# Performance work log

Measured on AMD Instinct MI355X. Metric: run time of the kernel, lower is better.

Reference implementation:

```python
import jax, jax.numpy as jnp
import numpy as np

N_EMBED = 384
HEAD_SIZE = 64
B, T = 128, 512


def rope(x):
    # Faithful to source: fres = 1/1000**(arange(0,dim,2)//dim) -> integer
    # floor-div makes the exponent all zeros, so fres == 1 everywhere.
    Bx, Tx, D = x.shape
    half = D // 2
    fres = jnp.ones((half,), dtype=jnp.float32)
    ang = jnp.arange(Tx, dtype=jnp.float32)[:, None] * fres[None, :]  # (T, half)
    cos, sin = jnp.cos(ang), jnp.sin(ang)
    xr = x.reshape(Bx, Tx, half, 2)
    xe, xo = xr[..., 0], xr[..., 1]
    oe = xe * cos - xo * sin
    oo = xe * sin + xo * cos
    return jnp.stack([oe, oo], axis=-1).reshape(Bx, Tx, D)


def setup_inputs() -> dict:
    key = jax.random.key(0)
    ks = jax.random.split(key, 7)
    s = 1.0 / np.sqrt(N_EMBED)
    return {
        "x": jax.random.normal(ks[0], (B, T, N_EMBED), dtype=jnp.float32),
        "wq": jax.random.uniform(ks[1], (N_EMBED, HEAD_SIZE), jnp.float32, -s, s),
        "bq": jax.random.uniform(ks[2], (HEAD_SIZE,), jnp.float32, -s, s),
        "wk": jax.random.uniform(ks[3], (N_EMBED, HEAD_SIZE), jnp.float32, -s, s),
        "bk": jax.random.uniform(ks[4], (HEAD_SIZE,), jnp.float32, -s, s),
        "wv": jax.random.uniform(ks[5], (N_EMBED, HEAD_SIZE), jnp.float32, -s, s),
        "bv": jax.random.uniform(ks[6], (HEAD_SIZE,), jnp.float32, -s, s),
    }


def reference(x, wq, bq, wk, bk, wv, bv):
    Bx, Tx, C = x.shape  # C = n_embed; scale uses C per the source (not head_size)
    q = rope(x @ wq + bq)
    k = rope(x @ wk + bk)
    wei = jnp.einsum("bqd,bkd->bqk", q, k) * (C ** -0.5)  # (B, T, T)
    causal = jnp.tril(jnp.ones((Tx, Tx), dtype=bool))
    wei = jnp.where(causal, wei, -jnp.inf)
    wei = jax.nn.softmax(wei, axis=-1)
    v = x @ wv + bv
    return jnp.einsum("bqk,bkd->bqd", wei, v)
```

## Files before the change

### kernel.cpp

```cpp
#include <hip/hip_runtime.h>

#define TSEQ 512
#define NB   128
#define CDIM 384
#define HD   64
#define QSCALE 0.051031036307982884f
#define MBIAS  8.0f

typedef _Float16 half8  __attribute__((ext_vector_type(8)));
typedef _Float16 half4  __attribute__((ext_vector_type(4)));
typedef float    floatx4 __attribute__((ext_vector_type(4)));

typedef __attribute__((address_space(3))) unsigned int lds_u32;
typedef const __attribute__((address_space(1))) unsigned int g_u32;

__device__ __forceinline__ void load_lds16(const void* g, void* l) {
    __builtin_amdgcn_global_load_lds((g_u32*)g, (lds_u32*)l, 16, 0, 0);
}

__global__ void prep_w(const float* __restrict__ wq, const float* __restrict__ wk,
                       const float* __restrict__ wv, _Float16* __restrict__ Wp)
{
    int i = blockIdx.x * 256 + threadIdx.x;
    if (i >= 3 * CDIM * HD) return;
    int c    = i / 6144;  int r  = i - c * 6144;
    int kblk = r / 1536;  int r2 = r - kblk * 1536;
    int n    = r2 >> 3;   int kin = r2 & 7;
    int k    = c * 32 + kblk * 8 + kin;
    int mat  = n / 64;    int col = n - mat * 64;
    const float* w = (mat == 0) ? wq : ((mat == 1) ? wk : wv);
    Wp[i] = (_Float16)w[k * HD + col];
}

__global__ __launch_bounds__(256, 4) void qkv_gemm(
    const float* __restrict__ x, const _Float16* __restrict__ Wp,
    const float* __restrict__ bq, const float* __restrict__ bk,
    const float* __restrict__ bv,
    _Float16* __restrict__ Qw, _Float16* __restrict__ Kw,
    _Float16* __restrict__ Vtw, int b0)
{
    __shared__ __align__(16) _Float16 wsb[3][6144];

    const int tid  = threadIdx.x;
    const int wave = tid >> 6;
    const int lane = tid & 63;
    const int l16  = lane & 15;
    const int quad = lane >> 4;

    const int row0 = blockIdx.x * 64;
    const size_t rowg = (size_t)b0 * TSEQ + row0;

    int woff[3];
#pragma unroll
    for (int i = 0; i < 3; ++i) woff[i] = (wave * 3 + i) * 512 + lane * 8;

    const float* xp = x + (rowg + wave * 16 + l16) * CDIM + quad * 8;

    floatx4 acc[12];
#pragma unroll
    for (int i = 0; i < 12; ++i)
#pragma unroll
        for (int r = 0; r < 4; ++r) acc[i][r] = 0.f;

    floatx4 xA[2], xB[2];

#define WSTAGE(cc) do { _Pragma("unroll")                                     \
    for (int i_ = 0; i_ < 3; ++i_)                                            \
        load_lds16(Wp + (size_t)(cc) * 6144 + woff[i_],                       \
                   (char*)&wsb[(cc) % 3][0] + (wave * 3 + i_) * 1024);        \
} while (0)

#define XLOAD(cc, S) do {                                                     \
    S[0] = *(const floatx4*)(xp + (cc) * 32);                                 \
    S[1] = *(const floatx4*)(xp + (cc) * 32 + 4);                             \
} while (0)

#define CHUNK(cc, CUR, NXT, VM) do {                                          \
    if ((cc) + 2 < 12) WSTAGE((cc) + 2);                                      \
    if ((cc) + 1 < 12) XLOAD((cc) + 1, NXT);                                  \
    asm volatile("s_waitcnt vmcnt(" VM ")" ::: "memory");                     \
    half8 aF;                                                                 \
    _Pragma("unroll")                                                         \
    for (int jj = 0; jj < 8; ++jj)                                            \
        aF[jj] = (_Float16)(jj < 4 ? CUR[0][jj] : CUR[1][jj - 4]);            \
    const _Float16* bp = &wsb[(cc) % 3][0] + ((size_t)quad * 192 + l16) * 8;  \
    _Pragma("unroll")                                                         \
    for (int i_ = 0; i_ < 12; ++i_) {                                         \
        half8 bb = *(const half8*)(bp + i_ * 128);                            \
        acc[i_] = __builtin_amdgcn_mfma_f32_16x16x32_f16(aF, bb, acc[i_], 0, 0, 0); \
    }                                                                         \
    __builtin_amdgcn_s_barrier();                                             \
} while (0)

    WSTAGE(0); WSTAGE(1); XLOAD(0, xA);
    asm volatile("s_waitcnt vmcnt(5)" ::: "memory");
    __builtin_amdgcn_s_barrier();

    CHUNK(0,  xA, xB, "5");  CHUNK(1,  xB, xA, "5");
    CHUNK(2,  xA, xB, "5");  CHUNK(3,  xB, xA, "5");
    CHUNK(4,  xA, xB, "5");  CHUNK(5,  xB, xA, "5");
    CHUNK(6,  xA, xB, "5");  CHUNK(7,  xB, xA, "5");
    CHUNK(8,  xA, xB, "5");  CHUNK(9,  xB, xA, "5");
    CHUNK(10, xA, xB, "2");  CHUNK(11, xB, xA, "0");

#undef CHUNK
#undef XLOAD
#undef WSTAGE

    float bq4[4], bk4[4], bv4[4];
#pragma unroll
    for (int s4 = 0; s4 < 4; ++s4) {
        const int cc = s4 * 16 + l16;
        bq4[s4] = bq[cc]; bk4[s4] = bk[cc]; bv4[s4] = bv[cc];
    }
    const int bidx = row0 >> 9;
    const int t00  = (row0 & (TSEQ - 1)) + wave * 16 + quad * 4;
    const int rowb = row0 + wave * 16 + quad * 4;

#pragma unroll
    for (int r = 0; r < 4; ++r) {
        const int t = t00 + r;
        const float st = sinf((float)t);
        const float ct = cosf((float)t);
        const int row = rowb + r;
#pragma unroll
        for (int s4 = 0; s4 < 4; ++s4) {
            const int cc = s4 * 16 + l16;
            float vq = acc[s4][r] + bq4[s4];
            float pq = __shfl_xor(vq, 1);
            vq = (cc & 1) ? (pq * st + vq * ct) : (vq * ct - pq * st);
            Qw[(size_t)row * HD + cc] = (_Float16)(vq * QSCALE);
            float vk = acc[4 + s4][r] + bk4[s4];
            float pk = __shfl_xor(vk, 1);
            vk = (cc & 1) ? (pk * st + vk * ct) : (vk * ct - pk * st);
            Kw[(size_t)row * HD + cc] = (_Float16)vk;
        }
    }
#pragma unroll
    for (int s4 = 0; s4 < 4; ++s4) {
        const int cc = s4 * 16 + l16;
        half4 vpack;
#pragma unroll
        for (int r = 0; r < 4; ++r) vpack[r] = (_Float16)(acc[8 + s4][r] + bv4[s4]);
        *(half4*)(Vtw + ((size_t)bidx * HD + cc) * TSEQ + t00) = vpack;
    }
}

__global__ __launch_bounds__(256, 3) void attn_kernel(
    const _Float16* __restrict__ Qw, const _Float16* __restrict__ Kw,
    const _Float16* __restrict__ Vtw, float* __restrict__ out, int b0)
{
    int bx, bl;
    {
        const int lin = blockIdx.y * 16 + blockIdx.x;
        if ((gridDim.y & 7) == 0) {
            const int per = gridDim.y >> 3;
            const int xcd = lin & 7;
            const int k2  = lin >> 3;
            bl = xcd * per + (k2 >> 4);
            bx = k2 & 15;
        } else { bx = blockIdx.x; bl = blockIdx.y; }
    }
    const int tid  = threadIdx.x;
    const int wave = tid >> 6;
    const int lane = tid & 63;
    const int l16  = lane & 15;
    const int quad = lane >> 4;

    const int pr  = bx;
    const int h   = wave;
    const int qA  = pr * 16;
    const int qB  = (31 - pr) * 16;
    const int jdA = pr >> 2;
    const int jdB = (31 - pr) >> 2;

    __shared__ __align__(16) _Float16 pbuf[4][16][72];
    __shared__ __align__(16) floatx4  mbuf[3][10][64];

    const _Float16* Qb = Qw  + (size_t)bl * TSEQ * HD;
    const _Float16* Kb = Kw  + (size_t)bl * TSEQ * HD;
    const _Float16* Vb = Vtw + (size_t)bl * HD * TSEQ;

    half8 aQA0 = *(const half8*)(Qb + (size_t)(qA + l16) * HD + quad * 8);
    half8 aQA1 = *(const half8*)(Qb + (size_t)(qA + l16) * HD + 32 + quad * 8);
    half8 aQB0 = *(const half8*)(Qb + (size_t)(qB + l16) * HD + quad * 8);
    half8 aQB1 = *(const half8*)(Qb + (size_t)(qB + l16) * HD + 32 + quad * 8);

    half8 ones;
#pragma unroll
    for (int jj = 0; jj < 8; ++jj) ones[jj] = (_Float16)1.f;

    floatx4 accO[8], accL[2];
#pragma unroll
    for (int i = 0; i < 8; ++i)
#pragma unroll
        for (int r = 0; r < 4; ++r) accO[i][r] = 0.f;
#pragma unroll
    for (int s = 0; s < 2; ++s)
#pragma unroll
        for (int r = 0; r < 4; ++r) accL[s][r] = 0.f;

    for (int j = h; j <= jdB; j += 4) {
        const int kb = j * 64;
        const bool actA = (j <= jdA);

        half8 bK0[4], bK1[4];
#pragma unroll
        for (int s4 = 0; s4 < 4; ++s4) {
            const _Float16* kp = Kb + (size_t)(kb + s4 * 16 + l16) * HD + quad * 8;
            bK0[s4] = *(const half8*)(kp);
            bK1[s4] = *(const half8*)(kp + 32);
        }

        if (actA) {
            floatx4 st4[4];
            __builtin_amdgcn_s_setprio(1);
#pragma unroll
            for (int s4 = 0; s4 < 4; ++s4) {
#pragma unroll
                for (int r = 0; r < 4; ++r) st4[s4][r] = 0.f;
                st4[s4] = __builtin_amdgcn_mfma_f32_16x16x32_f16(bK0[s4], aQA0, st4[s4], 0, 0, 0);
                st4[s4] = __builtin_amdgcn_mfma_f32_16x16x32_f16(bK1[s4], aQA1, st4[s4], 0, 0, 0);
            }
            __builtin_amdgcn_s_setprio(0);
            const int qrow = qA + l16;
#pragma unroll
            for (int s4 = 0; s4 < 4; ++s4) {
                half4 w;
#pragma unroll
                for (int r = 0; r < 4; ++r) {
                    float p = __expf(fminf(st4[s4][r], 18.f) - MBIAS);
                    if (j == jdA) {
                        const int kcol = kb + s4 * 16 + quad * 4 + r;
                        if (kcol > qrow) p = 0.f;
                    }
                    w[r] = (_Float16)p;
                }
                *(half4*)(&pbuf[wave][l16][s4 * 16 + quad * 4]) = w;
            }
        }

        floatx4 stB[4];
        __builtin_amdgcn_s_setprio(1);
#pragma unroll
        for (int s4 = 0; s4 < 4; ++s4) {
#pragma unroll
            for (int r = 0; r < 4; ++r) stB[s4][r] = 0.f;
            stB[s4] = __builtin_amdgcn_mfma_f32_16x16x32_f16(bK0[s4], aQB0, stB[s4], 0, 0, 0);
            stB[s4] = __builtin_amdgcn_mfma_f32_16x16x32_f16(bK1[s4], aQB1, stB[s4], 0, 0, 0);
        }
        __builtin_amdgcn_s_setprio(0);

        half8 bV0[4], bV1[4];
#pragma unroll
        for (int s4 = 0; s4 < 4; ++s4) {
            const _Float16* vp = Vb + (size_t)(s4 * 16 + l16) * TSEQ + kb + quad * 8;
            bV0[s4] = *(const half8*)(vp);
            bV1[s4] = *(const half8*)(vp + 32);
        }

        if (actA) {
            half8 aP0 = *(const half8*)(&pbuf[wave][l16][quad * 8]);
            half8 aP1 = *(const half8*)(&pbuf[wave][l16][32 + quad * 8]);
            __builtin_amdgcn_s_setprio(1);
#pragma unroll
            for (int s4 = 0; s4 < 4; ++s4) {
                accO[s4] = __builtin_amdgcn_mfma_f32_16x16x32_f16(aP0, bV0[s4], accO[s4], 0, 0, 0);
                accO[s4] = __builtin_amdgcn_mfma_f32_16x16x32_f16(aP1, bV1[s4], accO[s4], 0, 0, 0);
            }
            accL[0] = __builtin_amdgcn_mfma_f32_16x16x32_f16(aP0, ones, accL[0], 0, 0, 0);
            accL[0] = __builtin_amdgcn_mfma_f32_16x16x32_f16(aP1, ones, accL[0], 0, 0, 0);
            __builtin_amdgcn_s_setprio(0);
        }

        {
            const int qrow = qB + l16;
#pragma unroll
            for (int s4 = 0; s4 < 4; ++s4) {
                half4 w;
#pragma unroll
                for (int r = 0; r < 4; ++r) {
                    float p = __expf(fminf(stB[s4][r], 18.f) - MBIAS);
                    if (j == jdB) {
                        const int kcol = kb + s4 * 16 + quad * 4 + r;
                        if (kcol > qrow) p = 0.f;
                    }
                    w[r] = (_Float16)p;
                }
                *(half4*)(&pbuf[wave][l16][s4 * 16 + quad * 4]) = w;
            }
            half8 aP0 = *(const half8*)(&pbuf[wave][l16][quad * 8]);
            half8 aP1 = *(const half8*)(&pbuf[wave][l16][32 + quad * 8]);
            __builtin_amdgcn_s_setprio(1);
#pragma unroll
            for (int s4 = 0; s4 < 4; ++s4) {
                accO[4 + s4] = __builtin_amdgcn_mfma_f32_16x16x32_f16(aP0, bV0[s4], accO[4 + s4], 0, 0, 0);
                accO[4 + s4] = __builtin_amdgcn_mfma_f32_16x16x32_f16(aP1, bV1[s4], accO[4 + s4], 0, 0, 0);
            }
            accL[1] = __builtin_amdgcn_mfma_f32_16x16x32_f16(aP0, ones, accL[1], 0, 0, 0);
            accL[1] = __builtin_amdgcn_mfma_f32_16x16x32_f16(aP1, ones, accL[1], 0, 0, 0);
            __builtin_amdgcn_s_setprio(0);
        }
    }

    if (h != 0) {
#pragma unroll
        for (int i = 0; i < 8; ++i) mbuf[h - 1][i][lane] = accO[i];
        mbuf[h - 1][8][lane] = accL[0];
        mbuf[h - 1][9][lane] = accL[1];
    }
    __syncthreads();
    if (h != 0) return;

#pragma unroll
    for (int m = 0; m < 3; ++m) {
#pragma unroll
        for (int i = 0; i < 8; ++i) {
            floatx4 t = mbuf[m][i][lane];
#pragma unroll
            for (int r = 0; r < 4; ++r) accO[i][r] += t[r];
        }
        floatx4 t8 = mbuf[m][8][lane];
        floatx4 t9 = mbuf[m][9][lane];
#pragma unroll
        for (int r = 0; r < 4; ++r) { accL[0][r] += t8[r]; accL[1][r] += t9[r]; }
    }

#pragma unroll
    for (int s = 0; s < 2; ++s) {
        const int qbase = (s == 0) ? qA : qB;
        float inv[4];
#pragma unroll
        for (int r = 0; r < 4; ++r) inv[r] = 1.f / accL[s][r];
#pragma unroll
        for (int s4 = 0; s4 < 4; ++s4) {
            const int dcol = s4 * 16 + l16;
#pragma unroll
            for (int r = 0; r < 4; ++r) {
                const int qr = qbase + quad * 4 + r;
                out[((size_t)(b0 + bl) * TSEQ + qr) * HD + dcol] =
                    accO[s * 4 + s4][r] * inv[r];
            }
        }
    }
}

extern "C" void kernel_launch(void* const* d_in, const int* in_sizes, int n_in,
                              void* d_out, int out_size, void* d_ws, size_t ws_size,
                              hipStream_t stream)
{
    char* ws = (char*)d_ws;
    _Float16* Wp = (_Float16*)ws;
    char* qkv_base = ws + 147456;

    const size_t per_b = (size_t)3 * TSEQ * HD * sizeof(_Float16);
    size_t avail = (ws_size > (size_t)147456) ? ws_size - 147456 : per_b;
    int nbc = (int)(avail / per_b);
    if (nbc > NB) nbc = NB;
    if (nbc < 1)  nbc = 1;

    const size_t chunk_elems = (size_t)nbc * TSEQ * HD;
    _Float16* Qw  = (_Float16*)qkv_base;
    _Float16* Kw  = Qw + chunk_elems;
    _Float16* Vtw = Kw + chunk_elems;

    prep_w<<<dim3((3 * CDIM * HD + 255) / 256), dim3(256), 0, stream>>>(
        (const float*)d_in[1], (const float*)d_in[3], (const float*)d_in[5], Wp);

    for (int b0 = 0; b0 < NB; b0 += nbc) {
        const int nb = (NB - b0 < nbc) ? (NB - b0) : nbc;
        qkv_gemm<<<dim3(nb * 8), dim3(256), 0, stream>>>(
            (const float*)d_in[0], Wp, (const float*)d_in[2], (const float*)d_in[4],
            (const float*)d_in[6], Qw, Kw, Vtw, b0);
        attn_kernel<<<dim3(16, nb), dim3(256), 0, stream>>>(
            Qw, Kw, Vtw, (float*)d_out, b0);
    }
}
```

Measured before the change: 207.7 us.

## Load full QKV weight into LDS once per block and enlarge GEMM row tile

The QKV projection kernel now uses 512-thread blocks covering 256 rows each. Every block loads the whole fp16 weight matrix into LDS up front, about 144 KB, instead of streaming it in a triple-buffered ring with a barrier per chunk. Each wave computes two 16-row groups so every weight fragment read from LDS feeds two MFMAs, and x loads use a three-stage register rotation. This removes the per-chunk barriers and cuts weight traffic per row, but the large LDS footprint allows only one block per CU, the grid shrinks fourfold, and the doubled accumulators raise register pressure.

```diff
diff --git a/kernel.cpp b/kernel.cpp
--- a/kernel.cpp
+++ b/kernel.cpp
@@ -32,14 +32,14 @@
     Wp[i] = (_Float16)w[k * HD + col];
 }
 
-__global__ __launch_bounds__(256, 4) void qkv_gemm(
+__global__ __launch_bounds__(512) void qkv_gemm(
     const float* __restrict__ x, const _Float16* __restrict__ Wp,
     const float* __restrict__ bq, const float* __restrict__ bk,
     const float* __restrict__ bv,
     _Float16* __restrict__ Qw, _Float16* __restrict__ Kw,
     _Float16* __restrict__ Vtw, int b0)
 {
-    __shared__ __align__(16) _Float16 wsb[3][6144];
+    __shared__ __align__(16) _Float16 wsb[12][6144];
 
     const int tid  = threadIdx.x;
     const int wave = tid >> 6;
@@ -47,65 +47,66 @@
     const int l16  = lane & 15;
     const int quad = lane >> 4;
 
-    const int row0 = blockIdx.x * 64;
+    const int row0 = blockIdx.x * 256;
     const size_t rowg = (size_t)b0 * TSEQ + row0;
 
-    int woff[3];
-#pragma unroll
-    for (int i = 0; i < 3; ++i) woff[i] = (wave * 3 + i) * 512 + lane * 8;
-
-    const float* xp = x + (rowg + wave * 16 + l16) * CDIM + quad * 8;
-
-    floatx4 acc[12];
-#pragma unroll
-    for (int i = 0; i < 12; ++i)
-#pragma unroll
-        for (int r = 0; r < 4; ++r) acc[i][r] = 0.f;
-
-    floatx4 xA[2], xB[2];
-
-#define WSTAGE(cc) do { _Pragma("unroll")                                     \
-    for (int i_ = 0; i_ < 3; ++i_)                                            \
-        load_lds16(Wp + (size_t)(cc) * 6144 + woff[i_],                       \
-                   (char*)&wsb[(cc) % 3][0] + (wave * 3 + i_) * 1024);        \
+#pragma unroll
+    for (int i = 0; i < 18; ++i) {
+        const int I = wave * 18 + i;
+        load_lds16(Wp + (size_t)I * 512 + lane * 8, (char*)wsb + (size_t)I * 1024);
+    }
+
+    const float* xp[2];
+#pragma unroll
+    for (int g = 0; g < 2; ++g)
+        xp[g] = x + (rowg + wave * 32 + g * 16 + l16) * CDIM + quad * 8;
+
+    floatx4 acc[2][12];
+#pragma unroll
+    for (int g = 0; g < 2; ++g)
+#pragma unroll
+        for (int i = 0; i < 12; ++i)
+#pragma unroll
+            for (int r = 0; r < 4; ++r) acc[g][i][r] = 0.f;
+
+    floatx4 sA[2][2], sB[2][2], sC[2][2];
+
+#define XLOAD(cc, S) do { _Pragma("unroll")                                   \
+    for (int g_ = 0; g_ < 2; ++g_) {                                          \
+        S[g_][0] = *(const floatx4*)(xp[g_] + (cc) * 32);                     \
+        S[g_][1] = *(const floatx4*)(xp[g_] + (cc) * 32 + 4);                 \
+    }                                                                         \
 } while (0)
 
-#define XLOAD(cc, S) do {                                                     \
-    S[0] = *(const floatx4*)(xp + (cc) * 32);                                 \
-    S[1] = *(const floatx4*)(xp + (cc) * 32 + 4);                             \
-} while (0)
-
-#define CHUNK(cc, CUR, NXT, VM) do {                                          \
-    if ((cc) + 2 < 12) WSTAGE((cc) + 2);                                      \
-    if ((cc) + 1 < 12) XLOAD((cc) + 1, NXT);                                  \
-    asm volatile("s_waitcnt vmcnt(" VM ")" ::: "memory");                     \
-    half8 aF;                                                                 \
+#define CH(cc, CUR, NXT, lc) do {                                             \
+    if ((lc) < 12) XLOAD(lc, NXT);                                            \
+    half8 aF[2];                                                              \
     _Pragma("unroll")                                                         \
-    for (int jj = 0; jj < 8; ++jj)                                            \
-        aF[jj] = (_Float16)(jj < 4 ? CUR[0][jj] : CUR[1][jj - 4]);            \
-    const _Float16* bp = &wsb[(cc) % 3][0] + ((size_t)quad * 192 + l16) * 8;  \
+    for (int g_ = 0; g_ < 2; ++g_) {                                          \
+        _Pragma("unroll")                                                     \
+        for (int jj = 0; jj < 8; ++jj)                                        \
+            aF[g_][jj] = (_Float16)(jj < 4 ? CUR[g_][0][jj]                   \
+                                           : CUR[g_][1][jj - 4]);             \
+    }                                                                         \
+    const _Float16* bp = &wsb[cc][0] + ((size_t)quad * 192 + l16) * 8;        \
     _Pragma("unroll")                                                         \
     for (int i_ = 0; i_ < 12; ++i_) {                                         \
         half8 bb = *(const half8*)(bp + i_ * 128);                            \
-        acc[i_] = __builtin_amdgcn_mfma_f32_16x16x32_f16(aF, bb, acc[i_], 0, 0, 0); \
+        acc[0][i_] = __builtin_amdgcn_mfma_f32_16x16x32_f16(aF[0], bb, acc[0][i_], 0, 0, 0); \
+        acc[1][i_] = __builtin_amdgcn_mfma_f32_16x16x32_f16(aF[1], bb, acc[1][i_], 0, 0, 0); \
     }                                                                         \
-    __builtin_amdgcn_s_barrier();                                             \
 } while (0)
 
-    WSTAGE(0); WSTAGE(1); XLOAD(0, xA);
-    asm volatile("s_waitcnt vmcnt(5)" ::: "memory");
-    __builtin_amdgcn_s_barrier();
-
-    CHUNK(0,  xA, xB, "5");  CHUNK(1,  xB, xA, "5");
-    CHUNK(2,  xA, xB, "5");  CHUNK(3,  xB, xA, "5");
-    CHUNK(4,  xA, xB, "5");  CHUNK(5,  xB, xA, "5");
-    CHUNK(6,  xA, xB, "5");  CHUNK(7,  xB, xA, "5");
-    CHUNK(8,  xA, xB, "5");  CHUNK(9,  xB, xA, "5");
-    CHUNK(10, xA, xB, "2");  CHUNK(11, xB, xA, "0");
-
-#undef CHUNK
+    XLOAD(0, sA); XLOAD(1, sB);
+    __syncthreads();
+
+    CH(0,  sA, sC, 2);   CH(1,  sB, sA, 3);   CH(2,  sC, sB, 4);
+    CH(3,  sA, sC, 5);   CH(4,  sB, sA, 6);   CH(5,  sC, sB, 7);
+    CH(6,  sA, sC, 8);   CH(7,  sB, sA, 9);   CH(8,  sC, sB, 10);
+    CH(9,  sA, sC, 11);  CH(10, sB, sA, 12);  CH(11, sC, sB, 13);
+
+#undef CH
 #undef XLOAD
-#undef WSTAGE
 
     float bq4[4], bk4[4], bv4[4];
 #pragma unroll
@@ -114,35 +115,39 @@
         bq4[s4] = bq[cc]; bk4[s4] = bk[cc]; bv4[s4] = bv[cc];
     }
     const int bidx = row0 >> 9;
-    const int t00  = (row0 & (TSEQ - 1)) + wave * 16 + quad * 4;
-    const int rowb = row0 + wave * 16 + quad * 4;
-
-#pragma unroll
-    for (int r = 0; r < 4; ++r) {
-        const int t = t00 + r;
-        const float st = sinf((float)t);
-        const float ct = cosf((float)t);
-        const int row = rowb + r;
+
+#pragma unroll
+    for (int g = 0; g < 2; ++g) {
+        const int t00  = (row0 & (TSEQ - 1)) + wave * 32 + g * 16 + quad * 4;
+        const int rowb = row0 + wave * 32 + g * 16 + quad * 4;
+#pragma unroll
+        for (int r = 0; r < 4; ++r) {
+            const int t = t00 + r;
+            const float st = sinf((float)t);
+            const float ct = cosf((float)t);
+            const int row = rowb + r;
+#pragma unroll
+            for (int s4 = 0; s4 < 4; ++s4) {
+                const int cc = s4 * 16 + l16;
+                float vq = acc[g][s4][r] + bq4[s4];
+                float pq = __shfl_xor(vq, 1);
+                vq = (cc & 1) ? (pq * st + vq * ct) : (vq * ct - pq * st);
+                Qw[(size_t)row * HD + cc] = (_Float16)(vq * QSCALE);
+                float vk = acc[g][4 + s4][r] + bk4[s4];
+                float pk = __shfl_xor(vk, 1);
+                vk = (cc & 1) ? (pk * st + vk * ct) : (vk * ct - pk * st);
+                Kw[(size_t)row * HD + cc] = (_Float16)vk;
+            }
+        }
 #pragma unroll
         for (int s4 = 0; s4 < 4; ++s4) {
             const int cc = s4 * 16 + l16;
-            float vq = acc[s4][r] + bq4[s4];
-            float pq = __shfl_xor(vq, 1);
-            vq = (cc & 1) ? (pq * st + vq * ct) : (vq * ct - pq * st);
-            Qw[(size_t)row * HD + cc] = (_Float16)(vq * QSCALE);
-            float vk = acc[4 + s4][r] + bk4[s4];
-            float pk = __shfl_xor(vk, 1);
-            vk = (cc & 1) ? (pk * st + vk * ct) : (vk * ct - pk * st);
-            Kw[(size_t)row * HD + cc] = (_Float16)vk;
-        }
-    }
-#pragma unroll
-    for (int s4 = 0; s4 < 4; ++s4) {
-        const int cc = s4 * 16 + l16;
-        half4 vpack;
-#pragma unroll
-        for (int r = 0; r < 4; ++r) vpack[r] = (_Float16)(acc[8 + s4][r] + bv4[s4]);
-        *(half4*)(Vtw + ((size_t)bidx * HD + cc) * TSEQ + t00) = vpack;
+            half4 vpack;
+#pragma unroll
+            for (int r = 0; r < 4; ++r)
+                vpack[r] = (_Float16)(acc[g][8 + s4][r] + bv4[s4]);
+            *(half4*)(Vtw + ((size_t)bidx * HD + cc) * TSEQ + t00) = vpack;
+        }
     }
 }
 
@@ -369,7 +374,7 @@
 
     for (int b0 = 0; b0 < NB; b0 += nbc) {
         const int nb = (NB - b0 < nbc) ? (NB - b0) : nbc;
-        qkv_gemm<<<dim3(nb * 8), dim3(256), 0, stream>>>(
+        qkv_gemm<<<dim3(nb * 2), dim3(512), 0, stream>>>(
             (const float*)d_in[0], Wp, (const float*)d_in[2], (const float*)d_in[4],
             (const float*)d_in[6], Qw, Kw, Vtw, b0);
         attn_kernel<<<dim3(16, nb), dim3(256), 0, stream>>>(
```

Measured after the change: 219.9 us. +5.9%, slower.

## Prefetch whole x tile into LDS via async loads with smaller QKV blocks

Applied to the files above, without the earlier changes.

The QKV projection kernel now uses 128-thread blocks covering 32 rows and issues all twelve x chunks as asynchronous global-to-LDS loads up front. These go into a swizzled fp32 LDS buffer, replacing per-chunk register loads. Weight staging drops from triple to double buffering, with progressively decreasing vmcnt waits. The aim is deeper memory-level parallelism on the x stream and more blocks in flight. The cost is larger LDS use per block (48KB of x plus weights), an extra barrier per chunk, and twice the weight traffic per output row.

```diff
diff --git a/kernel.cpp b/kernel.cpp
--- a/kernel.cpp
+++ b/kernel.cpp
@@ -32,14 +32,15 @@
     Wp[i] = (_Float16)w[k * HD + col];
 }
 
-__global__ __launch_bounds__(256, 4) void qkv_gemm(
+__global__ __launch_bounds__(128) void qkv_gemm(
     const float* __restrict__ x, const _Float16* __restrict__ Wp,
     const float* __restrict__ bq, const float* __restrict__ bk,
     const float* __restrict__ bv,
     _Float16* __restrict__ Qw, _Float16* __restrict__ Kw,
     _Float16* __restrict__ Vtw, int b0)
 {
-    __shared__ __align__(16) _Float16 wsb[3][6144];
+    __shared__ __align__(16) float    xs[12 * 32 * 32];
+    __shared__ __align__(16) _Float16 wsb[2][6144];
 
     const int tid  = threadIdx.x;
     const int wave = tid >> 6;
@@ -47,14 +48,24 @@
     const int l16  = lane & 15;
     const int quad = lane >> 4;
 
-    const int row0 = blockIdx.x * 64;
+    const int row0 = blockIdx.x * 32;
     const size_t rowg = (size_t)b0 * TSEQ + row0;
 
-    int woff[3];
-#pragma unroll
-    for (int i = 0; i < 3; ++i) woff[i] = (wave * 3 + i) * 512 + lane * 8;
-
-    const float* xp = x + (rowg + wave * 16 + l16) * CDIM + quad * 8;
+    const float* xsrc[2];
+    int xdst[2];
+#pragma unroll
+    for (int i = 0; i < 2; ++i) {
+        const int t0 = (wave * 2 + i) * 64;
+        const int t  = t0 + lane;
+        const int m  = t >> 3;
+        const int u  = t & 7;
+        const int usw = u ^ (m & 7);
+        xsrc[i] = x + (rowg + m) * CDIM + usw * 4;
+        xdst[i] = t0 * 16;
+    }
+    int woff[6];
+#pragma unroll
+    for (int i = 0; i < 6; ++i) woff[i] = (wave * 6 + i) * 512 + lane * 8;
 
     floatx4 acc[12];
 #pragma unroll
@@ -62,49 +73,46 @@
 #pragma unroll
         for (int r = 0; r < 4; ++r) acc[i][r] = 0.f;
 
-    floatx4 xA[2], xB[2];
+#pragma unroll
+    for (int c = 0; c < 12; ++c)
+#pragma unroll
+        for (int i = 0; i < 2; ++i)
+            load_lds16(xsrc[i] + c * 32, (char*)xs + c * 4096 + xdst[i]);
 
 #define WSTAGE(cc) do { _Pragma("unroll")                                     \
-    for (int i_ = 0; i_ < 3; ++i_)                                            \
+    for (int i_ = 0; i_ < 6; ++i_)                                            \
         load_lds16(Wp + (size_t)(cc) * 6144 + woff[i_],                       \
-                   (char*)&wsb[(cc) % 3][0] + (wave * 3 + i_) * 1024);        \
+                   (char*)&wsb[(cc) & 1][0] + (wave * 6 + i_) * 1024);        \
 } while (0)
 
-#define XLOAD(cc, S) do {                                                     \
-    S[0] = *(const floatx4*)(xp + (cc) * 32);                                 \
-    S[1] = *(const floatx4*)(xp + (cc) * 32 + 4);                             \
-} while (0)
-
-#define CHUNK(cc, CUR, NXT, VM) do {                                          \
-    if ((cc) + 2 < 12) WSTAGE((cc) + 2);                                      \
-    if ((cc) + 1 < 12) XLOAD((cc) + 1, NXT);                                  \
+#define CHUNK(cc, VM) do {                                                    \
+    if ((cc) + 1 < 12) WSTAGE((cc) + 1);                                      \
     asm volatile("s_waitcnt vmcnt(" VM ")" ::: "memory");                     \
+    __builtin_amdgcn_s_barrier();       \
+    const int m_  = wave * 16 + l16;                                          \
+    const int mh_ = m_ & 7;                                                   \
+    const float* ap = xs + (cc) * 1024 + m_ * 32;                             \
+    floatx4 a0 = *(const floatx4*)(ap + (((quad * 2)     ^ mh_) << 2));       \
+    floatx4 a1 = *(const floatx4*)(ap + (((quad * 2 + 1) ^ mh_) << 2));       \
     half8 aF;                                                                 \
     _Pragma("unroll")                                                         \
     for (int jj = 0; jj < 8; ++jj)                                            \
-        aF[jj] = (_Float16)(jj < 4 ? CUR[0][jj] : CUR[1][jj - 4]);            \
-    const _Float16* bp = &wsb[(cc) % 3][0] + ((size_t)quad * 192 + l16) * 8;  \
+        aF[jj] = (_Float16)(jj < 4 ? a0[jj] : a1[jj - 4]);                    \
+    const _Float16* bp = &wsb[(cc) & 1][0] + ((size_t)quad * 192 + l16) * 8;  \
     _Pragma("unroll")                                                         \
     for (int i_ = 0; i_ < 12; ++i_) {                                         \
         half8 bb = *(const half8*)(bp + i_ * 128);                            \
         acc[i_] = __builtin_amdgcn_mfma_f32_16x16x32_f16(aF, bb, acc[i_], 0, 0, 0); \
     }                                                                         \
-    __builtin_amdgcn_s_barrier();                                             \
+    __builtin_amdgcn_s_barrier();      \
 } while (0)
 
-    WSTAGE(0); WSTAGE(1); XLOAD(0, xA);
-    asm volatile("s_waitcnt vmcnt(5)" ::: "memory");
-    __builtin_amdgcn_s_barrier();
-
-    CHUNK(0,  xA, xB, "5");  CHUNK(1,  xB, xA, "5");
-    CHUNK(2,  xA, xB, "5");  CHUNK(3,  xB, xA, "5");
-    CHUNK(4,  xA, xB, "5");  CHUNK(5,  xB, xA, "5");
-    CHUNK(6,  xA, xB, "5");  CHUNK(7,  xB, xA, "5");
-    CHUNK(8,  xA, xB, "5");  CHUNK(9,  xB, xA, "5");
-    CHUNK(10, xA, xB, "2");  CHUNK(11, xB, xA, "0");
+    WSTAGE(0);
+    CHUNK(0,  "28");  CHUNK(1,  "26");  CHUNK(2,  "24");  CHUNK(3,  "22");
+    CHUNK(4,  "20");  CHUNK(5,  "18");  CHUNK(6,  "16");  CHUNK(7,  "14");
+    CHUNK(8,  "12");  CHUNK(9,  "10");  CHUNK(10, "8");   CHUNK(11, "0");
 
 #undef CHUNK
-#undef XLOAD
 #undef WSTAGE
 
     float bq4[4], bk4[4], bv4[4];
@@ -369,7 +377,7 @@
 
     for (int b0 = 0; b0 < NB; b0 += nbc) {
         const int nb = (NB - b0 < nbc) ? (NB - b0) : nbc;
-        qkv_gemm<<<dim3(nb * 8), dim3(256), 0, stream>>>(
+        qkv_gemm<<<dim3(nb * 16), dim3(128), 0, stream>>>(
             (const float*)d_in[0], Wp, (const float*)d_in[2], (const float*)d_in[4],
             (const float*)d_in[6], Qw, Kw, Vtw, b0);
         attn_kernel<<<dim3(16, nb), dim3(256), 0, stream>>>(
```

After: 224.9 us. +8.3%, slower.
